# Kernel tuning notes

Measured on AMD Instinct MI355X. Metric: run time of the kernel, lower is better.

The kernel has to match this reference:

```python
import jax, jax.numpy as jnp
import numpy as np

B, C, N, K = 2, 128, 10000, 16


def setup_inputs() -> dict:
    key = jax.random.key(0)
    k1, k2, k3, k4 = jax.random.split(key, 4)
    x = jax.random.normal(k1, (B, C, N, 1), dtype=jnp.float32)
    edge_index = jax.random.randint(k2, (2, B, N, K), 0, N, dtype=jnp.int32)
    W = jax.random.normal(k3, (C, C), dtype=jnp.float32) * 0.05  # 1x1 conv C->C, no bias
    a = jax.random.normal(k4, (2 * C,), dtype=jnp.float32) * 0.05  # 1x1 conv 2C->1, no bias
    return {"x": x, "edge_index": edge_index, "W": W, "a": a}


def reference(x, edge_index, W, a):
    # x: [B,C,N,1], edge_index: [2,B,N,K]
    b, c, n, _ = x.shape
    k = edge_index.shape[-1]
    xs = x[..., 0]  # [B,C,N]
    wh = jnp.einsum('oc,bcn->bon', W, xs)  # 1x1 conv W(x): [B,C,N]
    # batched_index_select: gather along node dim -> [B,C,N,K]
    idx_i = edge_index[1].reshape(b, 1, n * k)
    idx_j = edge_index[0].reshape(b, 1, n * k)
    whi = jnp.take_along_axis(wh, idx_i, axis=2).reshape(b, c, n, k)
    whj = jnp.take_along_axis(wh, idx_j, axis=2).reshape(b, c, n, k)
    # a(cat([whi, whj], dim=1)) with a: 2C->1 == a_i . whi + a_j . whj
    e = jnp.einsum('c,bcnk->bnk', a[:c], whi) + jnp.einsum('c,bcnk->bnk', a[c:], whj)
    e = jax.nn.leaky_relu(e, negative_slope=0.2)
    A = jax.nn.softmax(e, axis=-1)  # [B,N,K]; dropout omitted (eval mode)
    h = jnp.einsum('bcnk,bnk->bcn', whj, A)  # mul + sum over K
    return h[..., None]  # [B,C,N,1]
```

## Files before the change

kernel.cpp:

```cpp
#include <hip/hip_runtime.h>


#define BB 2
#define CC 128
#define NN 10000
#define KK 16
#define TNG 64
#define TNA 16
#define LSTR 136

typedef unsigned int uint32;
typedef unsigned short ushort16_t;
typedef __attribute__((ext_vector_type(8))) short short8;
typedef __attribute__((ext_vector_type(4))) float floatx4;

__device__ __forceinline__ uint32 bf16pair(float lo, float hi) {
  uint32 ulo = __float_as_uint(lo);
  uint32 uhi = __float_as_uint(hi);
  ulo += 0x7fffu + ((ulo >> 16) & 1u);
  uhi += 0x7fffu + ((uhi >> 16) & 1u);
  return (ulo >> 16) | (uhi & 0xffff0000u);
}

__global__ __launch_bounds__(256) void gat_gemm(
    const float* __restrict__ x,
    const float* __restrict__ W,
    const float* __restrict__ a,
    uint32* __restrict__ wht,
    float* __restrict__ si,
    float* __restrict__ sj) {
  __shared__ ushort16_t Wl[CC * LSTR];
  __shared__ ushort16_t xs[TNG * LSTR];
  __shared__ float red[2][4][4][16];

  const int b  = blockIdx.y;
  const int n0 = blockIdx.x * TNG;
  const int t  = threadIdx.x;

  {
    const float2* Wg = (const float2*)W;
    uint32* Wd = (uint32*)Wl;
#pragma unroll
    for (int i = 0; i < 32; ++i) {
      int f2 = t + i * 256;
      float2 v = Wg[f2];
      int o = f2 >> 6, c2 = f2 & 63;
      Wd[o * 68 + c2] = bf16pair(v.x, v.y);
    }
  }
  {
    const float* xb = x + (size_t)b * CC * NN;
    uint32* xd = (uint32*)xs;
#pragma unroll
    for (int i = 0; i < 16; ++i) {
      int e = t + i * 256;
      int n = e & 63, cp = e >> 6;
      int c = cp * 2, gn = n0 + n;
      float v0 = 0.f, v1 = 0.f;
      if (gn < NN) { v0 = xb[c * NN + gn]; v1 = xb[(c + 1) * NN + gn]; }
      xd[n * 68 + cp] = bf16pair(v0, v1);
    }
  }
  __syncthreads();

  const int w    = t >> 6;
  const int lane = t & 63;
  const int col  = lane & 15;
  const int q    = lane >> 4;

  floatx4 acc[2][4];
#pragma unroll
  for (int ci = 0; ci < 2; ++ci)
#pragma unroll
    for (int nj = 0; nj < 4; ++nj) acc[ci][nj] = (floatx4){0.f, 0.f, 0.f, 0.f};

#pragma unroll
  for (int s = 0; s < 4; ++s) {
    const int ko = s * 32 + q * 8;
    short8 af[2], bf[4];
#pragma unroll
    for (int ci = 0; ci < 2; ++ci)
      af[ci] = *(const short8*)(Wl + (w * 32 + ci * 16 + col) * LSTR + ko);
#pragma unroll
    for (int nj = 0; nj < 4; ++nj)
      bf[nj] = *(const short8*)(xs + (nj * 16 + col) * LSTR + ko);
#pragma unroll
    for (int ci = 0; ci < 2; ++ci)
#pragma unroll
      for (int nj = 0; nj < 4; ++nj)
        acc[ci][nj] = __builtin_amdgcn_mfma_f32_16x16x32_bf16(af[ci], bf[nj], acc[ci][nj], 0, 0, 0);
  }

  float ar[2][4], aj4[2][4];
#pragma unroll
  for (int ci = 0; ci < 2; ++ci)
#pragma unroll
    for (int r = 0; r < 4; ++r) {
      int ch = w * 32 + ci * 16 + q * 4 + r;
      ar[ci][r]  = a[ch];
      aj4[ci][r] = a[CC + ch];
    }

#pragma unroll
  for (int nj = 0; nj < 4; ++nj) {
    int node = n0 + nj * 16 + col;
    float psi = 0.f, psj = 0.f;
#pragma unroll
    for (int ci = 0; ci < 2; ++ci) {
#pragma unroll
      for (int r = 0; r < 4; ++r) {
        psi = fmaf(ar[ci][r], acc[ci][nj][r], psi);
        psj = fmaf(aj4[ci][r], acc[ci][nj][r], psj);
      }
      if (node < NN) {
        uint2 pk;
        pk.x = bf16pair(acc[ci][nj][0], acc[ci][nj][1]);
        pk.y = bf16pair(acc[ci][nj][2], acc[ci][nj][3]);
        uint2* dst = (uint2*)(wht + ((size_t)(b * NN + node)) * (CC / 2) + w * 16 + ci * 8 + q * 2);
        *dst = pk;
      }
    }
    psi += __shfl_down(psi, 32);
    psi += __shfl_down(psi, 16);
    psj += __shfl_down(psj, 32);
    psj += __shfl_down(psj, 16);
    if (q == 0) { red[0][w][nj][col] = psi; red[1][w][nj][col] = psj; }
  }
  __syncthreads();

  if (t < TNG) {
    int gn = n0 + t;
    if (gn < NN) {
      int nj = t >> 4, cl = t & 15;
      float s1 = 0.f, s2 = 0.f;
#pragma unroll
      for (int ww = 0; ww < 4; ++ww) { s1 += red[0][ww][nj][cl]; s2 += red[1][ww][nj][cl]; }
      si[b * NN + gn] = s1;
      sj[b * NN + gn] = s2;
    }
  }
}

__global__ __launch_bounds__(256) void gat_gather(
    const int* __restrict__ ei,
    const uint32* __restrict__ wht,
    const float* __restrict__ si,
    const float* __restrict__ sj,
    float* __restrict__ out) {
  __shared__ float Am[TNA][KK];
  __shared__ int   jd[TNA][KK];
  __shared__ float outT[CC][TNA + 1];

  const int b  = blockIdx.y;
  const int n0 = blockIdx.x * TNA;
  const int t  = threadIdx.x;

  const int* eij = ei + b * NN * KK;
  const int* eii = ei + (BB + b) * NN * KK;
  const float* sib = si + b * NN;
  const float* sjb = sj + b * NN;

  {
    int nn = t >> 4, k = t & 15, gn = n0 + nn;
    float el = 0.f; int jj = 0;
    if (gn < NN) {
      jj = eij[gn * KK + k];
      int ii = eii[gn * KK + k];
      float v = sib[ii] + sjb[jj];
      el = (v > 0.f) ? v : 0.2f * v;
    }
    Am[nn][k] = el;
    jd[nn][k] = jj;
  }
  __syncthreads();

  if (t < TNA) {
    float mx = Am[t][0];
#pragma unroll
    for (int k = 1; k < KK; ++k) mx = fmaxf(mx, Am[t][k]);
    float s = 0.f, ex[KK];
#pragma unroll
    for (int k = 0; k < KK; ++k) { ex[k] = __expf(Am[t][k] - mx); s += ex[k]; }
    float inv = 1.f / s;
#pragma unroll
    for (int k = 0; k < KK; ++k) Am[t][k] = ex[k] * inv;
  }
  __syncthreads();

  const int cp = t & 63;
  const int nw = t >> 6;
  const uint32* whtb = wht + (size_t)b * NN * (CC / 2);
#pragma unroll
  for (int half = 0; half < 2; ++half) {
    int na = nw + half * 4;
    int idx[2][KK]; float wk[2][KK];
#pragma unroll
    for (int p = 0; p < 2; ++p) {
      int nn = na + p * 8;
      const uint4*   jp = (const uint4*)&jd[nn][0];
      const float4*  ap = (const float4*)&Am[nn][0];
#pragma unroll
      for (int g = 0; g < 4; ++g) {
        uint4  jv = jp[g];
        float4 av = ap[g];
        idx[p][4 * g + 0] = jv.x; idx[p][4 * g + 1] = jv.y;
        idx[p][4 * g + 2] = jv.z; idx[p][4 * g + 3] = jv.w;
        wk[p][4 * g + 0] = av.x;  wk[p][4 * g + 1] = av.y;
        wk[p][4 * g + 2] = av.z;  wk[p][4 * g + 3] = av.w;
      }
    }
    uint32 v[2][KK];
#pragma unroll
    for (int p = 0; p < 2; ++p)
#pragma unroll
      for (int k = 0; k < KK; ++k)
        v[p][k] = whtb[(size_t)idx[p][k] * (CC / 2) + cp];
#pragma unroll
    for (int p = 0; p < 2; ++p) {
      int nn = na + p * 8;
      float ax = 0.f, ay = 0.f;
#pragma unroll
      for (int k = 0; k < KK; ++k) {
        ax = fmaf(wk[p][k], __uint_as_float(v[p][k] << 16), ax);
        ay = fmaf(wk[p][k], __uint_as_float(v[p][k] & 0xffff0000u), ay);
      }
      outT[2 * cp][nn]     = ax;
      outT[2 * cp + 1][nn] = ay;
    }
  }
  __syncthreads();

  float* outb = out + (size_t)b * CC * NN;
#pragma unroll
  for (int i = 0; i < (CC * TNA) / 256; ++i) {
    int e = t + i * 256;
    int c = e >> 4, nn = e & 15;
    int gn = n0 + nn;
    if (gn < NN) outb[c * NN + gn] = outT[c][nn];
  }
}

extern "C" void kernel_launch(void* const* d_in, const int* in_sizes, int n_in,
                              void* d_out, int out_size, void* d_ws, size_t ws_size,
                              hipStream_t stream) {
  const float* x  = (const float*)d_in[0];
  const int*   ei = (const int*)d_in[1];
  const float* W  = (const float*)d_in[2];
  const float* a  = (const float*)d_in[3];
  float* out = (float*)d_out;

  uint32* wht = (uint32*)d_ws;
  float*  si  = (float*)(wht + (size_t)BB * NN * (CC / 2));
  float*  sj  = si + BB * NN;

  dim3 g1((NN + TNG - 1) / TNG, BB);
  dim3 g2((NN + TNA - 1) / TNA, BB);
  gat_gemm<<<g1, 256, 0, stream>>>(x, W, a, wht, si, sj);
  gat_gather<<<g2, 256, 0, stream>>>(ei, wht, si, sj, out);
}
```

Before: 88.19 us.

## Load W fragments directly into registers, halve GEMM tile, XCD-aware gather block mapping

The GEMM kernel no longer stages the full bf16 W matrix in LDS. Each wave loads its own W rows from global memory into MFMA A-fragment registers, and the node tile shrinks from 64 to 32, giving more blocks and a much smaller LDS footprint. The gather kernel switches to a 1D grid whose block index is remapped so that each batch's blocks land on a fixed subset of XCDs (4 per batch), so each batch's wht table stays within fewer L2 caches. The cost is redundant W global loads per block and a few idle padded blocks in the gather grid.

```diff
diff --git a/kernel.cpp b/kernel.cpp
--- a/kernel.cpp
+++ b/kernel.cpp
@@ -5,12 +5,11 @@
 #define CC 128
 #define NN 10000
 #define KK 16
-#define TNG 64
+#define TNG 32
 #define TNA 16
 #define LSTR 136
 
 typedef unsigned int uint32;
-typedef unsigned short ushort16_t;
 typedef __attribute__((ext_vector_type(8))) short short8;
 typedef __attribute__((ext_vector_type(4))) float floatx4;
 
@@ -29,66 +28,66 @@
     uint32* __restrict__ wht,
     float* __restrict__ si,
     float* __restrict__ sj) {
-  __shared__ ushort16_t Wl[CC * LSTR];
-  __shared__ ushort16_t xs[TNG * LSTR];
-  __shared__ float red[2][4][4][16];
-
-  const int b  = blockIdx.y;
-  const int n0 = blockIdx.x * TNG;
-  const int t  = threadIdx.x;
-
-  {
-    const float2* Wg = (const float2*)W;
-    uint32* Wd = (uint32*)Wl;
-#pragma unroll
-    for (int i = 0; i < 32; ++i) {
-      int f2 = t + i * 256;
-      float2 v = Wg[f2];
-      int o = f2 >> 6, c2 = f2 & 63;
-      Wd[o * 68 + c2] = bf16pair(v.x, v.y);
-    }
-  }
+  __shared__ unsigned short xs[TNG * LSTR];
+  __shared__ float red[2][4][2][16];
+
+  const int b    = blockIdx.y;
+  const int n0   = blockIdx.x * TNG;
+  const int t    = threadIdx.x;
+  const int w    = t >> 6;
+  const int lane = t & 63;
+  const int col  = lane & 15;
+  const int q    = lane >> 4;
+
   {
     const float* xb = x + (size_t)b * CC * NN;
     uint32* xd = (uint32*)xs;
 #pragma unroll
-    for (int i = 0; i < 16; ++i) {
+    for (int i = 0; i < 8; ++i) {
       int e = t + i * 256;
-      int n = e & 63, cp = e >> 6;
+      int n = e & 31, cp = e >> 5;
       int c = cp * 2, gn = n0 + n;
       float v0 = 0.f, v1 = 0.f;
       if (gn < NN) { v0 = xb[c * NN + gn]; v1 = xb[(c + 1) * NN + gn]; }
       xd[n * 68 + cp] = bf16pair(v0, v1);
     }
   }
-  __syncthreads();
-
-  const int w    = t >> 6;
-  const int lane = t & 63;
-  const int col  = lane & 15;
-  const int q    = lane >> 4;
-
-  floatx4 acc[2][4];
+
+  short8 af[2][4];
+#pragma unroll
+  for (int ci = 0; ci < 2; ++ci) {
+    const float* wr = W + (w * 32 + ci * 16 + col) * CC;
+#pragma unroll
+    for (int s = 0; s < 4; ++s) {
+      float4 f0 = *(const float4*)(wr + s * 32 + q * 8);
+      float4 f1 = *(const float4*)(wr + s * 32 + q * 8 + 4);
+      union { uint32 u[4]; short8 v; } cv;
+      cv.u[0] = bf16pair(f0.x, f0.y);
+      cv.u[1] = bf16pair(f0.z, f0.w);
+      cv.u[2] = bf16pair(f1.x, f1.y);
+      cv.u[3] = bf16pair(f1.z, f1.w);
+      af[ci][s] = cv.v;
+    }
+  }
+  __syncthreads();
+
+  floatx4 acc[2][2];
 #pragma unroll
   for (int ci = 0; ci < 2; ++ci)
 #pragma unroll
-    for (int nj = 0; nj < 4; ++nj) acc[ci][nj] = (floatx4){0.f, 0.f, 0.f, 0.f};
+    for (int nj = 0; nj < 2; ++nj) acc[ci][nj] = (floatx4){0.f, 0.f, 0.f, 0.f};
 
 #pragma unroll
   for (int s = 0; s < 4; ++s) {
-    const int ko = s * 32 + q * 8;
-    short8 af[2], bf[4];
+    short8 bf[2];
+#pragma unroll
+    for (int nj = 0; nj < 2; ++nj)
+      bf[nj] = *(const short8*)(xs + (nj * 16 + col) * LSTR + s * 32 + q * 8);
 #pragma unroll
     for (int ci = 0; ci < 2; ++ci)
-      af[ci] = *(const short8*)(Wl + (w * 32 + ci * 16 + col) * LSTR + ko);
-#pragma unroll
-    for (int nj = 0; nj < 4; ++nj)
-      bf[nj] = *(const short8*)(xs + (nj * 16 + col) * LSTR + ko);
-#pragma unroll
-    for (int ci = 0; ci < 2; ++ci)
-#pragma unroll
-      for (int nj = 0; nj < 4; ++nj)
-        acc[ci][nj] = __builtin_amdgcn_mfma_f32_16x16x32_bf16(af[ci], bf[nj], acc[ci][nj], 0, 0, 0);
+#pragma unroll
+      for (int nj = 0; nj < 2; ++nj)
+        acc[ci][nj] = __builtin_amdgcn_mfma_f32_16x16x32_bf16(af[ci][s], bf[nj], acc[ci][nj], 0, 0, 0);
   }
 
   float ar[2][4], aj4[2][4];
@@ -102,7 +101,7 @@
     }
 
 #pragma unroll
-  for (int nj = 0; nj < 4; ++nj) {
+  for (int nj = 0; nj < 2; ++nj) {
     int node = n0 + nj * 16 + col;
     float psi = 0.f, psj = 0.f;
 #pragma unroll
@@ -151,8 +150,12 @@
   __shared__ int   jd[TNA][KK];
   __shared__ float outT[CC][TNA + 1];
 
-  const int b  = blockIdx.y;
-  const int n0 = blockIdx.x * TNA;
+  const int bk   = blockIdx.x;
+  const int xcd  = bk & 7;
+  const int b    = xcd >> 2;
+  const int slot = (bk >> 3) * 4 + (xcd & 3);
+  if (slot >= (NN + TNA - 1) / TNA) return;
+  const int n0 = slot * TNA;
   const int t  = threadIdx.x;
 
   const int* eij = ei + b * NN * KK;
@@ -197,8 +200,8 @@
 #pragma unroll
     for (int p = 0; p < 2; ++p) {
       int nn = na + p * 8;
-      const uint4*   jp = (const uint4*)&jd[nn][0];
-      const float4*  ap = (const float4*)&Am[nn][0];
+      const uint4*  jp = (const uint4*)&jd[nn][0];
+      const float4* ap = (const float4*)&Am[nn][0];
 #pragma unroll
       for (int g = 0; g < 4; ++g) {
         uint4  jv = jp[g];
@@ -254,7 +257,6 @@
   float*  sj  = si + BB * NN;
 
   dim3 g1((NN + TNG - 1) / TNG, BB);
-  dim3 g2((NN + TNA - 1) / TNA, BB);
   gat_gemm<<<g1, 256, 0, stream>>>(x, W, a, wht, si, sj);
-  gat_gather<<<g2, 256, 0, stream>>>(ei, wht, si, sj, out);
-}
+  gat_gather<<<dim3(157 * 8), 256, 0, stream>>>(ei, wht, si, sj, out);
+}
```

Measured after the change: 87.35 us. Within noise of the previous version (-1.0%).
